# Performance work log

Measured on AMD Instinct MI355X. Metric: run time of the kernel, lower is better.

## Reference

```python
import jax, jax.numpy as jnp
import numpy as np

D_MODEL = 1024
N_HEAD = 16
D_HEAD = 64
BN, T = 4, 2048


def setup_inputs() -> dict:
    key = jax.random.key(0)
    k1, k2, k3, k4 = jax.random.split(key, 4)
    x = jax.random.normal(k1, (BN, T, D_MODEL), dtype=jnp.float32)
    mask = jax.random.randint(k2, (BN, T), 0, 2, dtype=jnp.int32)
    # to_qkv: Linear(d_model, 3*d_cat, bias=False); torch weight shape [out, in]
    w_qkv = jax.random.normal(k3, (3 * N_HEAD * D_HEAD, D_MODEL), dtype=jnp.float32) / np.sqrt(D_MODEL)
    w_tail = jax.random.normal(k4, (D_MODEL, N_HEAD * D_HEAD), dtype=jnp.float32) / np.sqrt(N_HEAD * D_HEAD)
    b_tail = jnp.zeros((D_MODEL,), dtype=jnp.float32)
    return {"x": x, "mask": mask, "w_qkv": w_qkv, "w_tail": w_tail, "b_tail": b_tail}


def reference(x, mask, w_qkv, w_tail, b_tail):
    bn, t, _ = x.shape
    scale = D_HEAD ** -0.5
    # qkv: [bn, t, 3*h*d] -> view(bn,t,h,3*d) -> chunk(3) along last dim
    qkv = jnp.einsum('btm,om->bto', x, w_qkv)
    qkv = qkv.reshape(bn, t, N_HEAD, 3, D_HEAD)  # chunk layout: [q|k|v] per head
    q = qkv[..., 0, :].transpose(0, 2, 1, 3)  # [bn, h, t, d]
    k = qkv[..., 1, :].transpose(0, 2, 1, 3)
    v = qkv[..., 2, :].transpose(0, 2, 1, 3)
    dots = jnp.einsum('bhqd,bhkd->bhqk', q, k) * scale  # [bn, h, t, t]
    keep = (mask != 0)[:, None, None, :]  # [bn, 1, 1, t]
    dots = jnp.where(keep, dots, -jnp.inf)
    coef = jax.nn.softmax(dots, axis=-1)  # dropout p=0 -> identity
    attn = jnp.einsum('bhqk,bhkd->bhqd', coef, v)
    out = attn.transpose(0, 2, 1, 3).reshape(bn, t, N_HEAD * D_HEAD)
    out = jnp.einsum('btc,oc->bto', out, w_tail) + b_tail
    return out
```

## Files before the change

### kernel.cpp

```cpp
#include <hip/hip_runtime.h>
#include <hip/hip_bf16.h>
#include <stdint.h>


typedef __attribute__((ext_vector_type(8))) short short8;
typedef __attribute__((ext_vector_type(4))) short short4b;
typedef __attribute__((ext_vector_type(4))) float f32x4;

#define T_SEQ 2048
#define NHEAD 16
#define DHEAD 64
#define DMODEL 1024

#if __has_builtin(__builtin_amdgcn_exp2f)
#define EXP2(x) __builtin_amdgcn_exp2f(x)
#else
#define EXP2(x) exp2f(x)
#endif

__device__ __forceinline__ ushort f2bf(float f) {
  __bf16 h = (__bf16)f;
  unsigned short u;
  __builtin_memcpy(&u, &h, 2);
  return u;
}
__device__ __forceinline__ float bf2f(ushort b) {
  return __uint_as_float(((uint32_t)b) << 16);
}

__device__ __forceinline__ int permInv(int x) {
  return (x & 0x23) | ((x & 0x0C) << 1) | ((x & 0x10) >> 2);
}

__device__ __forceinline__ void gload_lds16(const ushort* g, ushort* l) {
  __builtin_amdgcn_global_load_lds(
      (const __attribute__((address_space(1))) void*)g,
      (__attribute__((address_space(3))) void*)l, 16, 0, 0);
}

__global__ void cvt_all(const float* __restrict__ x,
                        const float* __restrict__ wq,
                        const float* __restrict__ wt,
                        ushort* __restrict__ out,
                        int n8x, int n8q, int n8t) {
  int i = blockIdx.x * blockDim.x + threadIdx.x;
  const float* src;
  int j;
  if (i < n8x) { src = x; j = i; }
  else if (i < n8x + n8q) { src = wq; j = i - n8x; }
  else if (i < n8x + n8q + n8t) { src = wt; j = i - n8x - n8q; }
  else return;
  const float4* p = (const float4*)(src + (size_t)j * 8);
  float4 a = p[0], b = p[1];
  short8 o;
  o[0] = (short)f2bf(a.x); o[1] = (short)f2bf(a.y);
  o[2] = (short)f2bf(a.z); o[3] = (short)f2bf(a.w);
  o[4] = (short)f2bf(b.x); o[5] = (short)f2bf(b.y);
  o[6] = (short)f2bf(b.z); o[7] = (short)f2bf(b.w);
  *(short8*)(out + (size_t)i * 8) = o;
}

template <int EPI>
__launch_bounds__(256)
__global__ void gemm_bt(const ushort* __restrict__ A,
                        const ushort* __restrict__ B,
                        void* __restrict__ Cout,
                        const float* __restrict__ bias,
                        const int* __restrict__ msk,
                        int M, int N, int K) {
  __shared__ ushort sA[2][128 * 64];
  __shared__ ushort sB[2][128 * 64];
  const int tid = threadIdx.x;
  const int lane = tid & 63;
  const int wid = tid >> 6;
  const int wr = wid >> 1, wc = wid & 1;
  const int bm = blockIdx.x * 128;
  const int bn = blockIdx.y * 128;
  const int l15 = lane & 15;
  const int lg = lane >> 4;

  f32x4 acc[4][4] = {};

  auto STAGE = [&](int buf, int k0) {
#pragma unroll
    for (int r = 0; r < 4; ++r) {
      int c = r * 256 + tid;
      int row = c >> 3, ci = c & 7;
      gload_lds16(A + (size_t)(bm + row) * K + k0 + ci * 8, &sA[buf][c * 8]);
      gload_lds16(B + (size_t)(bn + row) * K + k0 + ci * 8, &sB[buf][c * 8]);
    }
  };

  STAGE(0, 0);
  __syncthreads();

  const int nk = K >> 6;
  for (int kt = 0; kt < nk; ++kt) {
    const int cur = kt & 1;
    if (kt + 1 < nk) STAGE(cur ^ 1, (kt + 1) << 6);
#pragma unroll
    for (int ks = 0; ks < 2; ++ks) {
      short8 af[4], bfr[4];
#pragma unroll
      for (int m = 0; m < 4; ++m)
        af[m] = *(const short8*)&sA[cur][(wr * 64 + m * 16 + l15) * 64 + ks * 32 + lg * 8];
#pragma unroll
      for (int n = 0; n < 4; ++n)
        bfr[n] = *(const short8*)&sB[cur][(wc * 64 + n * 16 + l15) * 64 + ks * 32 + lg * 8];
      __builtin_amdgcn_s_setprio(1);
#pragma unroll
      for (int m = 0; m < 4; ++m)
#pragma unroll
        for (int n = 0; n < 4; ++n)
          acc[m][n] = __builtin_amdgcn_mfma_f32_16x16x32_bf16(af[m], bfr[n], acc[m][n], 0, 0, 0);
      __builtin_amdgcn_s_setprio(0);
    }
    __syncthreads();
  }

  if (EPI == 0) {
    ushort* qkvb = (ushort*)Cout;
    const int b = bm >> 11;
    int mk[4][4];
#pragma unroll
    for (int m = 0; m < 4; ++m)
#pragma unroll
      for (int r = 0; r < 4; ++r) {
        int gr = bm + wr * 64 + m * 16 + lg * 4 + r;
        mk[m][r] = msk[b * T_SEQ + (gr & (T_SEQ - 1))];
      }
#pragma unroll
    for (int m = 0; m < 4; ++m)
#pragma unroll
      for (int n = 0; n < 4; ++n)
#pragma unroll
        for (int r = 0; r < 4; ++r) {
          int gr = bm + wr * 64 + m * 16 + lg * 4 + r;
          int gc = bn + wc * 64 + n * 16 + l15;
          int t = gr & (T_SEQ - 1);
          int h = gc / 192, rem = gc - h * 192;
          int sel = rem >> 6, d = rem & 63;
          size_t base = (size_t)((b * NHEAD + h) * 3 + sel) * T_SEQ * DHEAD;
          float v = acc[m][n][r];
          size_t dst;
          if (sel == 2) {
            int tp = (t & ~63) | permInv(t & 63);
            if (!mk[m][r]) v = 0.f;
            dst = base + (size_t)d * T_SEQ + tp;
          } else {
            dst = base + (size_t)t * DHEAD + d;
          }
          qkvb[dst] = f2bf(v);
        }
  } else {
    float* out = (float*)Cout;
#pragma unroll
    for (int m = 0; m < 4; ++m)
#pragma unroll
      for (int n = 0; n < 4; ++n) {
        int gc = bn + wc * 64 + n * 16 + l15;
        float bv = bias[gc];
#pragma unroll
        for (int r = 0; r < 4; ++r) {
          int gr = bm + wr * 64 + m * 16 + lg * 4 + r;
          out[(size_t)gr * N + gc] = acc[m][n][r] + bv;
        }
      }
  }
}

__launch_bounds__(256)
__global__ void attn_fwd(const ushort* __restrict__ qkv,
                         const int* __restrict__ mask,
                         ushort* __restrict__ attn) {
  __shared__ ushort sK[3][64 * 64];
  __shared__ ushort sVT[3][64 * 64];
  __shared__ ushort sInd[T_SEQ];

  const int tid = threadIdx.x;
  const int lane = tid & 63;
  const int wid = tid >> 6;
  const int l15 = lane & 15;
  const int lg = lane >> 4;
  const int bid = blockIdx.x;
  const int qt = (bid >> 3) & 15;
  const int bh = ((bid >> 7) << 3) | (bid & 7);
  const int b = bh >> 4, h = bh & 15;

  const ushort* Qp  = qkv + (size_t)(bh * 3 + 0) * T_SEQ * DHEAD;
  const ushort* Kp  = qkv + (size_t)(bh * 3 + 1) * T_SEQ * DHEAD;
  const ushort* VTp = qkv + (size_t)(bh * 3 + 2) * T_SEQ * DHEAD;
  const int* mrow = mask + b * T_SEQ;

  const int qbase = qt * 128 + wid * 32;

#pragma unroll
  for (int e = 0; e < 8; ++e) {
    int kv = tid * 8 + e;
    int p = (kv & ~63) | permInv(kv & 63);
    sInd[p] = mrow[kv] ? (ushort)0x3F80 : (ushort)0;
  }

  const float QSCALE = 0.18033688011112042f;
  short8 qf[2][2];
#pragma unroll
  for (int m = 0; m < 2; ++m)
#pragma unroll
    for (int ks = 0; ks < 2; ++ks) {
      short8 raw = *(const short8*)&Qp[(size_t)(qbase + m * 16 + l15) * 64 + ks * 32 + lg * 8];
#pragma unroll
      for (int e = 0; e < 8; ++e)
        qf[m][ks][e] = (short)f2bf(bf2f((ushort)raw[e]) * QSCALE);
    }

  f32x4 lacc[2] = {};
  f32x4 oacc[2][4] = {};

  auto STAGE = [&](int buf, int kt) {
    const int kb = kt * 64;
#pragma unroll
    for (int r2 = 0; r2 < 2; ++r2) {
      int c = r2 * 256 + tid;
      int row = c >> 3, ci = c & 7;
      int sb = (ci ^ (row & 7)) * 8;
      gload_lds16(Kp + (size_t)(kb + row) * 64 + sb, &sK[buf][c * 8]);
      gload_lds16(VTp + (size_t)row * T_SEQ + kb + sb, &sVT[buf][c * 8]);
    }
  };

  auto QKT = [&](int bufi, f32x4 (*st)[2]) {
    short8 kf0[4], kf1[4];
#pragma unroll
    for (int n = 0; n < 4; ++n) {
      kf0[n] = *(const short8*)&sK[bufi][(n * 16 + l15) * 64 + (((0 + lg) ^ (l15 & 7)) * 8)];
      kf1[n] = *(const short8*)&sK[bufi][(n * 16 + l15) * 64 + (((4 + lg) ^ (l15 & 7)) * 8)];
    }
    __builtin_amdgcn_s_setprio(1);
#pragma unroll
    for (int n = 0; n < 4; ++n)
#pragma unroll
      for (int m = 0; m < 2; ++m) {
        f32x4 z = {0.f, 0.f, 0.f, 0.f};
        st[n][m] = __builtin_amdgcn_mfma_f32_16x16x32_bf16(kf0[n], qf[m][0], z, 0, 0, 0);
        st[n][m] = __builtin_amdgcn_mfma_f32_16x16x32_bf16(kf1[n], qf[m][1], st[n][m], 0, 0, 0);
      }
    __builtin_amdgcn_s_setprio(0);
  };

  const int NT = T_SEQ / 64;

#define ATT_HALF(STC, STN, T, BC, BN_, BS)                                   \
  {                                                                          \
    _Pragma("unroll")                                                        \
    for (int m = 0; m < 2; ++m)                                              \
      _Pragma("unroll")                                                      \
      for (int n = 0; n < 4; ++n)                                            \
        _Pragma("unroll")                                                    \
        for (int r = 0; r < 4; ++r)                                          \
          STC[n][m][r] = EXP2(STC[n][m][r]);                                 \
    short8 pa[2][2];                                                         \
    _Pragma("unroll")                                                        \
    for (int m = 0; m < 2; ++m)                                              \
      _Pragma("unroll")                                                      \
      for (int ks = 0; ks < 2; ++ks)                                         \
        _Pragma("unroll")                                                    \
        for (int e = 0; e < 4; ++e) {                                        \
          pa[m][ks][e]     = (short)f2bf(STC[ks * 2][m][e]);                 \
          pa[m][ks][4 + e] = (short)f2bf(STC[ks * 2 + 1][m][e]);             \
        }                                                                    \
    asm volatile("s_waitcnt vmcnt(0)" ::: "memory");                         \
    __builtin_amdgcn_sched_barrier(0);                                       \
    __builtin_amdgcn_s_barrier();                                            \
    if ((T) + 2 < NT) STAGE(BS, (T) + 2);                                    \
    if ((T) + 1 < NT) QKT(BN_, STN);                                         \
    _Pragma("unroll")                                                        \
    for (int ks = 0; ks < 2; ++ks) {                                         \
      short8 vf[4];                                                          \
      _Pragma("unroll")                                                      \
      for (int dt = 0; dt < 4; ++dt)                                         \
        vf[dt] = *(const short8*)&sVT[BC][(dt * 16 + l15) * 64 +             \
                 (((ks * 4 + lg) ^ (l15 & 7)) * 8)];                         \
      short8 vi = *(const short8*)&sInd[(T) * 64 + ks * 32 + lg * 8];        \
      __builtin_amdgcn_s_setprio(1);                                         \
      _Pragma("unroll")                                                      \
      for (int dt = 0; dt < 4; ++dt)                                         \
        _Pragma("unroll")                                                    \
        for (int m = 0; m < 2; ++m)                                          \
          oacc[m][dt] = __builtin_amdgcn_mfma_f32_16x16x32_bf16(             \
              vf[dt], pa[m][ks], oacc[m][dt], 0, 0, 0);                      \
      _Pragma("unroll")                                                      \
      for (int m = 0; m < 2; ++m)                                            \
        lacc[m] = __builtin_amdgcn_mfma_f32_16x16x32_bf16(                   \
            vi, pa[m][ks], lacc[m], 0, 0, 0);                                \
      __builtin_amdgcn_s_setprio(0);                                         \
    }                                                                        \
  }

  STAGE(0, 0);
  STAGE(1, 1);
  __syncthreads();

  f32x4 stA[4][2], stB[4][2];
  QKT(0, stA);

  int cur = 0;
  for (int kt = 0; kt < NT; kt += 2) {
    int b1 = cur + 1; if (b1 >= 3) b1 -= 3;
    int b2 = cur + 2; if (b2 >= 3) b2 -= 3;
    ATT_HALF(stA, stB, kt,     cur, b1, b2);
    ATT_HALF(stB, stA, kt + 1, b1,  b2, cur);
    cur = b2;
  }
#undef ATT_HALF

#pragma unroll
  for (int m = 0; m < 2; ++m) {
    float rl = 1.0f / lacc[m][0];
    int t = qbase + m * 16 + l15;
#pragma unroll
    for (int dt = 0; dt < 4; ++dt) {
      short4b ov;
#pragma unroll
      for (int r = 0; r < 4; ++r) ov[r] = (short)f2bf(oacc[m][dt][r] * rl);
      *(short4b*)&attn[(size_t)(b * T_SEQ + t) * DMODEL + h * DHEAD + dt * 16 + lg * 4] = ov;
    }
  }
}

extern "C" void kernel_launch(void* const* d_in, const int* in_sizes, int n_in,
                              void* d_out, int out_size, void* d_ws, size_t ws_size,
                              hipStream_t stream) {
  (void)in_sizes; (void)n_in; (void)out_size; (void)ws_size;
  const float* x      = (const float*)d_in[0];
  const int*   mask   = (const int*)d_in[1];
  const float* w_qkv  = (const float*)d_in[2];
  const float* w_tail = (const float*)d_in[3];
  const float* b_tail = (const float*)d_in[4];
  float* out = (float*)d_out;

  const size_t M = 4 * 2048;
  ushort* xb     = (ushort*)d_ws;
  ushort* wqkvb  = xb + M * DMODEL;
  ushort* wtailb = wqkvb + 3 * DMODEL * DMODEL;
  ushort* qkvb   = wtailb + DMODEL * DMODEL;
  ushort* attnb  = qkvb + (size_t)64 * 3 * T_SEQ * DHEAD;

  {
    int n8x = (int)(M * DMODEL / 8);
    int n8q = 3 * DMODEL * DMODEL / 8;
    int n8t = DMODEL * DMODEL / 8;
    int n8 = n8x + n8q + n8t;
    cvt_all<<<(n8 + 255) / 256, 256, 0, stream>>>(x, w_qkv, w_tail, xb, n8x, n8q, n8t);
  }

  gemm_bt<0><<<dim3(M / 128, 3 * DMODEL / 128), 256, 0, stream>>>(
      xb, wqkvb, qkvb, nullptr, mask, (int)M, 3 * DMODEL, DMODEL);

  attn_fwd<<<dim3(1024), 256, 0, stream>>>(qkvb, mask, attnb);

  gemm_bt<1><<<dim3(M / 128, DMODEL / 128), 256, 0, stream>>>(
      attnb, wtailb, out, b_tail, nullptr, (int)M, DMODEL, DMODEL);
}
```

Before: 210.5 us.

## Use 256x256-tile 8-wave GEMM with swizzled LDS for QKV projection

Replaces the 128x128 QKV projection GEMM with a dedicated 512-thread kernel computing 256x256 tiles. It uses direct global-to-LDS loads with an XOR swizzle, a phased double-buffered schedule that interleaves loads with MFMA blocks, and an XCD-aware remap of block indices. The larger tile raises arithmetic intensity and cuts redundant global traffic. In exchange it needs a lot of LDS and registers (one block per CU), and the grid gets smaller (384 blocks). The output projection GEMM is simplified to a non-templated version.

```diff
diff --git a/kernel.cpp b/kernel.cpp
--- a/kernel.cpp
+++ b/kernel.cpp
@@ -60,13 +60,158 @@
   *(short8*)(out + (size_t)i * 8) = o;
 }
 
-template <int EPI>
+__launch_bounds__(512, 1)
+__global__ void gemm256_qkv(const ushort* __restrict__ A,
+                            const ushort* __restrict__ B,
+                            ushort* __restrict__ qkvb,
+                            const int* __restrict__ msk,
+                            int M, int N, int K) {
+  __shared__ ushort sA[2][2][128 * 64];
+  __shared__ ushort sB[2][2][128 * 64];
+
+  const int tid = threadIdx.x;
+  const int lane = tid & 63;
+  const int wid = tid >> 6;
+  const int wm = wid >> 2;
+  const int wn = wid & 3;
+  const int l15 = lane & 15;
+  const int lg = lane >> 4;
+  const int swz = l15 & 7;
+
+  const int nwg_x = N >> 8;
+  const int cpx = (M >> 8) * nwg_x / 8;
+  const int wg = (blockIdx.x & 7) * cpx + (blockIdx.x >> 3);
+  const int bm = (wg / nwg_x) << 8;
+  const int bn = (wg % nwg_x) << 8;
+
+  f32x4 acc[8][4] = {};
+
+  auto STG = [&](ushort* dst, const ushort* srcRow0, int kt) {
+#pragma unroll
+    for (int r = 0; r < 2; ++r) {
+      int c = r * 512 + tid;
+      int row = c >> 3, ci = c & 7;
+      int sb = (ci ^ (row & 7)) * 8;
+      gload_lds16(srcRow0 + (size_t)row * K + kt * 64 + sb, dst + c * 8);
+    }
+  };
+  const ushort* Abase[2] = {A + (size_t)bm * K, A + (size_t)(bm + 128) * K};
+  const ushort* Bbase[2] = {B + (size_t)bn * K, B + (size_t)(bn + 128) * K};
+
+#define PHASE(BUFC, Q, CC)                                                   \
+  do {                                                                       \
+    short8 af[4][2], bfr[2][2];                                              \
+    _Pragma("unroll")                                                        \
+    for (int fr = 0; fr < 4; ++fr)                                           \
+      _Pragma("unroll")                                                      \
+      for (int ks = 0; ks < 2; ++ks) {                                       \
+        int row = (Q) * 64 + fr * 16 + l15;                                  \
+        int ch = (ks * 4 + lg) ^ swz;                                        \
+        af[fr][ks] = *(const short8*)&sA[BUFC][wm][row * 64 + ch * 8];       \
+      }                                                                      \
+    _Pragma("unroll")                                                        \
+    for (int fc = 0; fc < 2; ++fc)                                           \
+      _Pragma("unroll")                                                      \
+      for (int ks = 0; ks < 2; ++ks) {                                       \
+        int ci2 = wn * 64 + (CC) * 32 + fc * 16 + l15;                       \
+        int ch = (ks * 4 + lg) ^ swz;                                        \
+        bfr[fc][ks] =                                                        \
+            *(const short8*)&sB[BUFC][ci2 >> 7][(ci2 & 127) * 64 + ch * 8];  \
+      }                                                                      \
+    asm volatile("s_barrier" ::: "memory");                                  \
+    __builtin_amdgcn_s_setprio(1);                                           \
+    _Pragma("unroll")                                                        \
+    for (int fr = 0; fr < 4; ++fr)                                           \
+      _Pragma("unroll")                                                      \
+      for (int fc = 0; fc < 2; ++fc)                                         \
+        _Pragma("unroll")                                                    \
+        for (int ks = 0; ks < 2; ++ks)                                       \
+          acc[(Q) * 4 + fr][(CC) * 2 + fc] =                                 \
+              __builtin_amdgcn_mfma_f32_16x16x32_bf16(                       \
+                  af[fr][ks], bfr[fc][ks], acc[(Q) * 4 + fr][(CC) * 2 + fc], \
+                  0, 0, 0);                                                  \
+    __builtin_amdgcn_s_setprio(0);                                           \
+    asm volatile("s_barrier" ::: "memory");                                  \
+  } while (0)
+
+  STG(&sA[0][0][0], Abase[0], 0);
+  STG(&sA[0][1][0], Abase[1], 0);
+  STG(&sB[0][0][0], Bbase[0], 0);
+  STG(&sB[0][1][0], Bbase[1], 0);
+  asm volatile("s_waitcnt vmcnt(0)" ::: "memory");
+  __builtin_amdgcn_sched_barrier(0);
+  asm volatile("s_barrier" ::: "memory");
+
+  const int nkt = K >> 6;
+  for (int it = 0; it < (nkt >> 1); ++it) {
+    const int T = it * 2;
+    asm volatile("s_waitcnt vmcnt(0)" ::: "memory");
+    __builtin_amdgcn_sched_barrier(0);
+    asm volatile("s_barrier" ::: "memory");
+    STG(&sA[1][0][0], Abase[0], T + 1);
+    STG(&sB[1][0][0], Bbase[0], T + 1);
+    PHASE(0, 0, 0);
+    STG(&sA[1][1][0], Abase[1], T + 1);
+    STG(&sB[1][1][0], Bbase[1], T + 1);
+    PHASE(0, 1, 0);
+    PHASE(0, 0, 1);
+    PHASE(0, 1, 1);
+    asm volatile("s_waitcnt vmcnt(0)" ::: "memory");
+    __builtin_amdgcn_sched_barrier(0);
+    asm volatile("s_barrier" ::: "memory");
+    if (T + 2 < nkt) {
+      STG(&sA[0][0][0], Abase[0], T + 2);
+      STG(&sB[0][0][0], Bbase[0], T + 2);
+    }
+    PHASE(1, 0, 0);
+    if (T + 2 < nkt) {
+      STG(&sA[0][1][0], Abase[1], T + 2);
+      STG(&sB[0][1][0], Bbase[1], T + 2);
+    }
+    PHASE(1, 1, 0);
+    PHASE(1, 0, 1);
+    PHASE(1, 1, 1);
+  }
+#undef PHASE
+
+  const int b = bm >> 11;
+#pragma unroll
+  for (int ar = 0; ar < 8; ++ar) {
+    int mk[4];
+#pragma unroll
+    for (int rr = 0; rr < 4; ++rr) {
+      int gr = bm + wm * 128 + ar * 16 + lg * 4 + rr;
+      mk[rr] = msk[b * T_SEQ + (gr & (T_SEQ - 1))];
+    }
+#pragma unroll
+    for (int ac = 0; ac < 4; ++ac)
+#pragma unroll
+      for (int rr = 0; rr < 4; ++rr) {
+        int gr = bm + wm * 128 + ar * 16 + lg * 4 + rr;
+        int gc = bn + wn * 64 + ac * 16 + l15;
+        int t = gr & (T_SEQ - 1);
+        int h = gc / 192, rem = gc - h * 192;
+        int sel = rem >> 6, d = rem & 63;
+        size_t base = (size_t)((b * NHEAD + h) * 3 + sel) * T_SEQ * DHEAD;
+        float v = acc[ar][ac][rr];
+        size_t dst;
+        if (sel == 2) {
+          int tp = (t & ~63) | permInv(t & 63);
+          if (!mk[rr]) v = 0.f;
+          dst = base + (size_t)d * T_SEQ + tp;
+        } else {
+          dst = base + (size_t)t * DHEAD + d;
+        }
+        qkvb[dst] = f2bf(v);
+      }
+  }
+}
+
 __launch_bounds__(256)
 __global__ void gemm_bt(const ushort* __restrict__ A,
                         const ushort* __restrict__ B,
-                        void* __restrict__ Cout,
+                        float* __restrict__ Cout,
                         const float* __restrict__ bias,
-                        const int* __restrict__ msk,
                         int M, int N, int K) {
   __shared__ ushort sA[2][128 * 64];
   __shared__ ushort sB[2][128 * 64];
@@ -118,55 +263,18 @@
     __syncthreads();
   }
 
-  if (EPI == 0) {
-    ushort* qkvb = (ushort*)Cout;
-    const int b = bm >> 11;
-    int mk[4][4];
-#pragma unroll
-    for (int m = 0; m < 4; ++m)
+#pragma unroll
+  for (int m = 0; m < 4; ++m)
+#pragma unroll
+    for (int n = 0; n < 4; ++n) {
+      int gc = bn + wc * 64 + n * 16 + l15;
+      float bv = bias[gc];
 #pragma unroll
       for (int r = 0; r < 4; ++r) {
         int gr = bm + wr * 64 + m * 16 + lg * 4 + r;
-        mk[m][r] = msk[b * T_SEQ + (gr & (T_SEQ - 1))];
+        Cout[(size_t)gr * N + gc] = acc[m][n][r] + bv;
       }
-#pragma unroll
-    for (int m = 0; m < 4; ++m)
-#pragma unroll
-      for (int n = 0; n < 4; ++n)
-#pragma unroll
-        for (int r = 0; r < 4; ++r) {
-          int gr = bm + wr * 64 + m * 16 + lg * 4 + r;
-          int gc = bn + wc * 64 + n * 16 + l15;
-          int t = gr & (T_SEQ - 1);
-          int h = gc / 192, rem = gc - h * 192;
-          int sel = rem >> 6, d = rem & 63;
-          size_t base = (size_t)((b * NHEAD + h) * 3 + sel) * T_SEQ * DHEAD;
-          float v = acc[m][n][r];
-          size_t dst;
-          if (sel == 2) {
-            int tp = (t & ~63) | permInv(t & 63);
-            if (!mk[m][r]) v = 0.f;
-            dst = base + (size_t)d * T_SEQ + tp;
-          } else {
-            dst = base + (size_t)t * DHEAD + d;
-          }
-          qkvb[dst] = f2bf(v);
-        }
-  } else {
-    float* out = (float*)Cout;
-#pragma unroll
-    for (int m = 0; m < 4; ++m)
-#pragma unroll
-      for (int n = 0; n < 4; ++n) {
-        int gc = bn + wc * 64 + n * 16 + l15;
-        float bv = bias[gc];
-#pragma unroll
-        for (int r = 0; r < 4; ++r) {
-          int gr = bm + wr * 64 + m * 16 + lg * 4 + r;
-          out[(size_t)gr * N + gc] = acc[m][n][r] + bv;
-        }
-      }
-  }
+    }
 }
 
 __launch_bounds__(256)
@@ -353,11 +461,11 @@
     cvt_all<<<(n8 + 255) / 256, 256, 0, stream>>>(x, w_qkv, w_tail, xb, n8x, n8q, n8t);
   }
 
-  gemm_bt<0><<<dim3(M / 128, 3 * DMODEL / 128), 256, 0, stream>>>(
-      xb, wqkvb, qkvb, nullptr, mask, (int)M, 3 * DMODEL, DMODEL);
+  gemm256_qkv<<<dim3((M / 256) * (3 * DMODEL / 256)), 512, 0, stream>>>(
+      xb, wqkvb, qkvb, mask, (int)M, 3 * DMODEL, DMODEL);
 
   attn_fwd<<<dim3(1024), 256, 0, stream>>>(qkvb, mask, attnb);
 
-  gemm_bt<1><<<dim3(M / 128, DMODEL / 128), 256, 0, stream>>>(
-      attnb, wtailb, out, b_tail, nullptr, (int)M, DMODEL, DMODEL);
-}
+  gemm_bt<<<dim3(M / 128, DMODEL / 128), 256, 0, stream>>>(
+      attnb, wtailb, out, b_tail, (int)M, DMODEL, DMODEL);
+}
```

Result: slower. 237.1 us (+12.7%).

## Rewrite projection GEMMs with 256x128 tiles, triple-buffered LDS, and swizzle

Applied to the files above, without the earlier changes.

Both projection GEMMs now use 512-thread blocks computing 256x128 tiles with eight waves. K-tiles are triple-buffered using explicit vmcnt waits and one barrier per iteration, with XOR-swizzled LDS layouts to avoid bank conflicts. Workgroup IDs are remapped across groups of 8 to improve L2 locality. The aim is better MFMA utilisation and overlap of loads with compute. The cost is much more LDS per block (about 144KB), which limits occupancy to one block per CU.

```diff
diff --git a/kernel.cpp b/kernel.cpp
--- a/kernel.cpp
+++ b/kernel.cpp
@@ -61,109 +61,145 @@
 }
 
 template <int EPI>
-__launch_bounds__(256)
-__global__ void gemm_bt(const ushort* __restrict__ A,
-                        const ushort* __restrict__ B,
-                        void* __restrict__ Cout,
-                        const float* __restrict__ bias,
-                        const int* __restrict__ msk,
-                        int M, int N, int K) {
-  __shared__ ushort sA[2][128 * 64];
-  __shared__ ushort sB[2][128 * 64];
+__launch_bounds__(512, 1)
+__global__ void gemm3b(const ushort* __restrict__ A,
+                       const ushort* __restrict__ B,
+                       void* __restrict__ Cout,
+                       const float* __restrict__ bias,
+                       const int* __restrict__ msk,
+                       int M, int N, int K) {
+  __shared__ ushort sA[3][256 * 64];
+  __shared__ ushort sB[3][128 * 64];
+
   const int tid = threadIdx.x;
   const int lane = tid & 63;
   const int wid = tid >> 6;
-  const int wr = wid >> 1, wc = wid & 1;
-  const int bm = blockIdx.x * 128;
-  const int bn = blockIdx.y * 128;
+  const int wm = wid >> 2;
+  const int wn = wid & 3;
   const int l15 = lane & 15;
   const int lg = lane >> 4;
-
-  f32x4 acc[4][4] = {};
-
-  auto STAGE = [&](int buf, int k0) {
+  const int swz = l15 & 7;
+
+  const int nbn = N >> 7;
+  const int nwg = (M >> 8) * nbn;
+  const int cpx = nwg >> 3;
+  const int wg = (blockIdx.x & 7) * cpx + (blockIdx.x >> 3);
+  const int bm = (wg / nbn) << 8;
+  const int bn = (wg % nbn) << 7;
+
+  f32x4 acc[8][2] = {};
+
+  auto STAGE = [&](int buf, int kt) {
 #pragma unroll
     for (int r = 0; r < 4; ++r) {
-      int c = r * 256 + tid;
+      int c = r * 512 + tid;
       int row = c >> 3, ci = c & 7;
-      gload_lds16(A + (size_t)(bm + row) * K + k0 + ci * 8, &sA[buf][c * 8]);
-      gload_lds16(B + (size_t)(bn + row) * K + k0 + ci * 8, &sB[buf][c * 8]);
+      int sb = (ci ^ (row & 7)) * 8;
+      gload_lds16(A + (size_t)(bm + row) * K + kt * 64 + sb, &sA[buf][c * 8]);
+    }
+#pragma unroll
+    for (int r = 0; r < 2; ++r) {
+      int c = r * 512 + tid;
+      int row = c >> 3, ci = c & 7;
+      int sb = (ci ^ (row & 7)) * 8;
+      gload_lds16(B + (size_t)(bn + row) * K + kt * 64 + sb, &sB[buf][c * 8]);
     }
   };
 
+  const int nkt = K >> 6;
   STAGE(0, 0);
-  __syncthreads();
-
-  const int nk = K >> 6;
-  for (int kt = 0; kt < nk; ++kt) {
-    const int cur = kt & 1;
-    if (kt + 1 < nk) STAGE(cur ^ 1, (kt + 1) << 6);
-#pragma unroll
-    for (int ks = 0; ks < 2; ++ks) {
-      short8 af[4], bfr[4];
-#pragma unroll
-      for (int m = 0; m < 4; ++m)
-        af[m] = *(const short8*)&sA[cur][(wr * 64 + m * 16 + l15) * 64 + ks * 32 + lg * 8];
-#pragma unroll
-      for (int n = 0; n < 4; ++n)
-        bfr[n] = *(const short8*)&sB[cur][(wc * 64 + n * 16 + l15) * 64 + ks * 32 + lg * 8];
+  STAGE(1, 1);
+
+  int bufT = 0;
+  for (int kt = 0; kt < nkt; ++kt) {
+    if (kt + 1 < nkt) {
+      asm volatile("s_waitcnt vmcnt(6)" ::: "memory");
+    } else {
+      asm volatile("s_waitcnt vmcnt(0)" ::: "memory");
+    }
+    __builtin_amdgcn_sched_barrier(0);
+    __builtin_amdgcn_s_barrier();
+    __builtin_amdgcn_sched_barrier(0);
+    if (kt + 2 < nkt) {
+      int nb = bufT + 2; if (nb >= 3) nb -= 3;
+      STAGE(nb, kt + 2);
+    }
+
+    short8 bfr[2][2];
+#pragma unroll
+    for (int fc = 0; fc < 2; ++fc)
+#pragma unroll
+      for (int ks = 0; ks < 2; ++ks)
+        bfr[fc][ks] = *(const short8*)&sB[bufT][(wn * 32 + fc * 16 + l15) * 64 +
+                                               ((ks * 4 + lg) ^ swz) * 8];
+#pragma unroll
+    for (int QQ = 0; QQ < 2; ++QQ) {
+      short8 af[4][2];
+#pragma unroll
+      for (int fr = 0; fr < 4; ++fr)
+#pragma unroll
+        for (int ks = 0; ks < 2; ++ks)
+          af[fr][ks] = *(const short8*)&sA[bufT][(wm * 128 + (QQ * 4 + fr) * 16 + l15) * 64 +
+                                                ((ks * 4 + lg) ^ swz) * 8];
       __builtin_amdgcn_s_setprio(1);
 #pragma unroll
-      for (int m = 0; m < 4; ++m)
-#pragma unroll
-        for (int n = 0; n < 4; ++n)
-          acc[m][n] = __builtin_amdgcn_mfma_f32_16x16x32_bf16(af[m], bfr[n], acc[m][n], 0, 0, 0);
+      for (int fr = 0; fr < 4; ++fr)
+#pragma unroll
+        for (int fc = 0; fc < 2; ++fc)
+#pragma unroll
+          for (int ks = 0; ks < 2; ++ks)
+            acc[QQ * 4 + fr][fc] = __builtin_amdgcn_mfma_f32_16x16x32_bf16(
+                af[fr][ks], bfr[fc][ks], acc[QQ * 4 + fr][fc], 0, 0, 0);
       __builtin_amdgcn_s_setprio(0);
     }
-    __syncthreads();
+    bufT = (bufT + 1 == 3) ? 0 : bufT + 1;
   }
 
   if (EPI == 0) {
     ushort* qkvb = (ushort*)Cout;
     const int b = bm >> 11;
-    int mk[4][4];
-#pragma unroll
-    for (int m = 0; m < 4; ++m)
-#pragma unroll
-      for (int r = 0; r < 4; ++r) {
-        int gr = bm + wr * 64 + m * 16 + lg * 4 + r;
-        mk[m][r] = msk[b * T_SEQ + (gr & (T_SEQ - 1))];
+#pragma unroll
+    for (int ar = 0; ar < 8; ++ar) {
+      int mk[4];
+#pragma unroll
+      for (int rr = 0; rr < 4; ++rr) {
+        int gr = bm + wm * 128 + ar * 16 + lg * 4 + rr;
+        mk[rr] = msk[b * T_SEQ + (gr & (T_SEQ - 1))];
       }
 #pragma unroll
-    for (int m = 0; m < 4; ++m)
-#pragma unroll
-      for (int n = 0; n < 4; ++n)
-#pragma unroll
-        for (int r = 0; r < 4; ++r) {
-          int gr = bm + wr * 64 + m * 16 + lg * 4 + r;
-          int gc = bn + wc * 64 + n * 16 + l15;
+      for (int ac = 0; ac < 2; ++ac)
+#pragma unroll
+        for (int rr = 0; rr < 4; ++rr) {
+          int gr = bm + wm * 128 + ar * 16 + lg * 4 + rr;
+          int gc = bn + wn * 32 + ac * 16 + l15;
           int t = gr & (T_SEQ - 1);
           int h = gc / 192, rem = gc - h * 192;
           int sel = rem >> 6, d = rem & 63;
           size_t base = (size_t)((b * NHEAD + h) * 3 + sel) * T_SEQ * DHEAD;
-          float v = acc[m][n][r];
+          float v = acc[ar][ac][rr];
           size_t dst;
           if (sel == 2) {
             int tp = (t & ~63) | permInv(t & 63);
-            if (!mk[m][r]) v = 0.f;
+            if (!mk[rr]) v = 0.f;
             dst = base + (size_t)d * T_SEQ + tp;
           } else {
             dst = base + (size_t)t * DHEAD + d;
           }
           qkvb[dst] = f2bf(v);
         }
+    }
   } else {
     float* out = (float*)Cout;
 #pragma unroll
-    for (int m = 0; m < 4; ++m)
-#pragma unroll
-      for (int n = 0; n < 4; ++n) {
-        int gc = bn + wc * 64 + n * 16 + l15;
+    for (int ar = 0; ar < 8; ++ar)
+#pragma unroll
+      for (int ac = 0; ac < 2; ++ac) {
+        int gc = bn + wn * 32 + ac * 16 + l15;
         float bv = bias[gc];
 #pragma unroll
-        for (int r = 0; r < 4; ++r) {
-          int gr = bm + wr * 64 + m * 16 + lg * 4 + r;
-          out[(size_t)gr * N + gc] = acc[m][n][r] + bv;
+        for (int rr = 0; rr < 4; ++rr) {
+          int gr = bm + wm * 128 + ar * 16 + lg * 4 + rr;
+          out[(size_t)gr * N + gc] = acc[ar][ac][rr] + bv;
         }
       }
   }
@@ -353,11 +389,11 @@
     cvt_all<<<(n8 + 255) / 256, 256, 0, stream>>>(x, w_qkv, w_tail, xb, n8x, n8q, n8t);
   }
 
-  gemm_bt<0><<<dim3(M / 128, 3 * DMODEL / 128), 256, 0, stream>>>(
+  gemm3b<0><<<dim3((M / 256) * (3 * DMODEL / 128)), 512, 0, stream>>>(
       xb, wqkvb, qkvb, nullptr, mask, (int)M, 3 * DMODEL, DMODEL);
 
   attn_fwd<<<dim3(1024), 256, 0, stream>>>(qkvb, mask, attnb);
 
-  gemm_bt<1><<<dim3(M / 128, DMODEL / 128), 256, 0, stream>>>(
+  gemm3b<1><<<dim3((M / 256) * (DMODEL / 128)), 512, 0, stream>>>(
       attnb, wtailb, out, b_tail, nullptr, (int)M, DMODEL, DMODEL);
 }
```

Measured after the change: 215.7 us. +2.5%, slower.
